# Optimization experiments

Measured on AMD Instinct MI355X. Metric: run time of the kernel, lower is better.

## Reference

```python
import jax, jax.numpy as jnp
import numpy as np

NUM_HEADS = 8
DIM_NODE, DIM_EDGE, DIM_TIME, DIM_OUT = 512, 172, 100, 512
U_NODE, U_EDGE, U_TIME, NUM_DST, E = 100000, 8192, 50000, 16384, 131072


def _linear_params(k, fan_in, fan_out):
    # torch.nn.Linear default init: U(-1/sqrt(fan_in), 1/sqrt(fan_in))
    kw, kb = jax.random.split(k)
    bound = 1.0 / np.sqrt(fan_in)
    w = jax.random.uniform(kw, (fan_in, fan_out), jnp.float32, -bound, bound)
    b = jax.random.uniform(kb, (fan_out,), jnp.float32, -bound, bound)
    return w, b


def setup_inputs() -> dict:
    key = jax.random.key(0)
    ks = jax.random.split(key, 16)
    inp = {}
    inp["idx"] = jax.random.randint(ks[0], (E,), 0, NUM_DST, jnp.int32)
    inp["nodeData"] = jax.random.normal(ks[1], (U_NODE, DIM_NODE), jnp.float32)
    inp["node_inverse"] = jax.random.randint(ks[2], (E,), 0, U_NODE, jnp.int32)
    inp["node_dst_inverse"] = jax.random.randint(ks[3], (NUM_DST,), 0, U_NODE, jnp.int32)
    inp["efeat_unique"] = jax.random.normal(ks[4], (U_EDGE, DIM_EDGE), jnp.float32)
    inp["efeat_inverse"] = jax.random.randint(ks[5], (E,), 0, U_EDGE, jnp.int32)
    inp["time_unique"] = jax.random.normal(ks[6], (U_TIME, DIM_TIME), jnp.float32)
    inp["time_inverse"] = jax.random.randint(ks[7], (E,), 0, U_TIME, jnp.int32)
    inp["time_dst_unique"] = jax.random.normal(ks[8], (1, DIM_TIME), jnp.float32)
    inp["time_dst_inverse"] = jnp.zeros((NUM_DST,), jnp.int32)
    inp["wq_node_w"], inp["wq_node_b"] = _linear_params(ks[9], DIM_NODE, DIM_OUT)
    inp["wq_time_w"], inp["wq_time_b"] = _linear_params(ks[10], DIM_TIME, DIM_OUT)
    inp["wkv_node_w"], inp["wkv_node_b"] = _linear_params(ks[11], DIM_NODE, 2 * DIM_OUT)
    inp["wkv_edge_w"], inp["wkv_edge_b"] = _linear_params(ks[12], DIM_EDGE, 2 * DIM_OUT)
    inp["wkv_time_w"], inp["wkv_time_b"] = _linear_params(ks[13], DIM_TIME, 2 * DIM_OUT)
    return inp


def reference(idx, nodeData, node_inverse, node_dst_inverse, efeat_unique,
              efeat_inverse, time_unique, time_inverse, time_dst_unique,
              time_dst_inverse, wq_node_w, wq_node_b, wq_time_w, wq_time_b,
              wkv_node_w, wkv_node_b, wkv_edge_w, wkv_edge_b, wkv_time_w,
              wkv_time_b):
    # project on UNIQUE rows, then scatter via inverse indices (dedup pattern)
    q_node = (nodeData @ wq_node_w + wq_node_b)[node_dst_inverse]      # [num_dst, D]
    q_time = (time_dst_unique @ wq_time_w + wq_time_b)[time_dst_inverse]
    Q = (q_node + q_time)[idx]                                          # [E, D]
    z_node = (nodeData @ wkv_node_w + wkv_node_b)[node_inverse]         # [E, 2D]
    z_edge = (efeat_unique @ wkv_edge_w + wkv_edge_b)[efeat_inverse]
    z_time = (time_unique @ wkv_time_w + wkv_time_b)[time_inverse]
    Z = z_node + z_edge + z_time
    D = wq_node_w.shape[1]
    K, V = Z[:, :D], Z[:, D:]
    n = Q.shape[0]
    Qh = Q.reshape(n, NUM_HEADS, -1)
    Kh = K.reshape(n, NUM_HEADS, -1)
    Vh = V.reshape(n, NUM_HEADS, -1)
    attn = jnp.sum(Qh * Kh, axis=2)                                      # [E, H]
    attn = jnp.where(attn >= 0, attn, 0.2 * attn)                        # LeakyReLU(0.2)
    return attn, Vh
```

## Files before the change

### kernel.cpp

```cpp
#include <hip/hip_runtime.h>
#include <hip/hip_bf16.h>

typedef __bf16 bf16_t;
typedef __bf16 bf16x8 __attribute__((ext_vector_type(8)));
typedef float  f32x4  __attribute__((ext_vector_type(4)));

#define E_NUM   131072
#define NDST    16384
#define DN      512
#define DE      172
#define DEP     192
#define DT      100
#define DTP     128
#define DO      512
#define KTOT    832
#define VBASE   (E_NUM * 8)

typedef const __attribute__((address_space(1))) char gbl_t;
typedef __attribute__((address_space(3))) char lds_t;

#define GLOAD_LDS16(g, l) __builtin_amdgcn_global_load_lds((gbl_t*)(g), (lds_t*)(l), 16, 0, 0)

__global__ void cvt_bf16_vec(const float* __restrict__ src, bf16_t* __restrict__ dst, long n8) {
    long i = (long)blockIdx.x * blockDim.x + threadIdx.x;
    long stride = (long)gridDim.x * blockDim.x;
    for (; i < n8; i += stride) {
        const float4* p = reinterpret_cast<const float4*>(src + i * 8);
        float4 a = p[0], b = p[1];
        union { bf16_t h[8]; uint4 q; } t;
        t.h[0]=(bf16_t)a.x; t.h[1]=(bf16_t)a.y; t.h[2]=(bf16_t)a.z; t.h[3]=(bf16_t)a.w;
        t.h[4]=(bf16_t)b.x; t.h[5]=(bf16_t)b.y; t.h[6]=(bf16_t)b.z; t.h[7]=(bf16_t)b.w;
        *reinterpret_cast<uint4*>(dst + i * 8) = t.q;
    }
}

__global__ void cvt_pad(const float* __restrict__ src, bf16_t* __restrict__ dst,
                        int rows, int cin, int cout) {
    long total = (long)rows * cout;
    long i = (long)blockIdx.x * blockDim.x + threadIdx.x;
    long stride = (long)gridDim.x * blockDim.x;
    for (; i < total; i += stride) {
        int r = (int)(i / cout), c = (int)(i - (long)r * cout);
        dst[i] = (c < cin) ? (bf16_t)src[(size_t)r * cin + c] : (bf16_t)0.0f;
    }
}

__global__ void prep_wkvT(const float* __restrict__ wn, const float* __restrict__ we,
                          const float* __restrict__ wt, const float* __restrict__ bn,
                          const float* __restrict__ be, const float* __restrict__ bt,
                          bf16_t* __restrict__ WkvT, float* __restrict__ kvbias) {
    int n = blockIdx.x;
    for (int k = threadIdx.x; k < KTOT; k += blockDim.x) {
        float v;
        if (k < 512)            v = wn[(size_t)k * 1024 + n];
        else if (k < 512 + DE)  v = we[(size_t)(k - 512) * 1024 + n];
        else if (k < 704)       v = 0.0f;
        else if (k < 704 + DT)  v = wt[(size_t)(k - 704) * 1024 + n];
        else                    v = 0.0f;
        WkvT[(size_t)n * KTOT + k] = (bf16_t)v;
    }
    if (threadIdx.x == 0) kvbias[n] = bn[n] + be[n] + bt[n];
}

__global__ void prep_wqT(const float* __restrict__ wq, bf16_t* __restrict__ WqT) {
    int n = blockIdx.x;
    for (int k = threadIdx.x; k < DO; k += blockDim.x)
        WqT[(size_t)n * DO + k] = (bf16_t)wq[(size_t)k * DO + n];
}

__global__ void prep_qbias(const float* __restrict__ td, const float* __restrict__ wqt,
                           const float* __restrict__ bqt, const float* __restrict__ bqn,
                           float* __restrict__ qbias) {
    int n = blockIdx.x * blockDim.x + threadIdx.x;
    if (n < DO) {
        float s = bqt[n] + bqn[n];
        for (int k = 0; k < DT; ++k) s += td[k] * wqt[(size_t)k * DO + n];
        qbias[n] = s;
    }
}

__global__ __launch_bounds__(256) void qd_gemm_kernel(
    const bf16_t* __restrict__ node_bf, const int* __restrict__ node_dst,
    const bf16_t* __restrict__ WqT, const float* __restrict__ qbias,
    float* __restrict__ QD) {
    const int bx = blockIdx.x;
    const int mt = bx >> 2, nt = bx & 3;
    const int d0 = mt * 128, n0 = nt * 128;
    const int tid = threadIdx.x;
    const int lane = tid & 63, wid = tid >> 6;
    const int wm = wid >> 1, wn = wid & 1;
    const int lr = lane & 15, lg = lane >> 4;

    __shared__ __align__(16) bf16_t Ash[2][128 * 32];
    __shared__ __align__(16) bf16_t Bsh[2][128 * 32];

    const int srow = wid * 32 + (lane >> 2);
    const int achk = lane & 3;
    const bf16_t* pa0 = node_bf + (size_t)node_dst[d0 + srow] * DN + achk * 8;
    const bf16_t* pa1 = node_bf + (size_t)node_dst[d0 + srow + 16] * DN + achk * 8;
    const bf16_t* pb0 = WqT + (size_t)(n0 + srow) * DO + achk * 8;
    const bf16_t* pb1 = pb0 + (size_t)16 * DO;

#define QD_STAGE(buf, kt) do {                                                   \
        int k0_ = (kt) * 32;                                                     \
        GLOAD_LDS16(pa0 + k0_, &Ash[buf][0] + wid * 1024);                       \
        GLOAD_LDS16(pa1 + k0_, &Ash[buf][0] + wid * 1024 + 512);                 \
        GLOAD_LDS16(pb0 + k0_, &Bsh[buf][0] + wid * 1024);                       \
        GLOAD_LDS16(pb1 + k0_, &Bsh[buf][0] + wid * 1024 + 512);                 \
    } while (0)

    f32x4 acc[4][4];
#pragma unroll
    for (int i = 0; i < 4; ++i)
#pragma unroll
        for (int j = 0; j < 4; ++j) { acc[i][j][0]=0.f; acc[i][j][1]=0.f; acc[i][j][2]=0.f; acc[i][j][3]=0.f; }

    QD_STAGE(0, 0);
    __syncthreads();
    int cur = 0;
    for (int kt = 0; kt < 16; ++kt) {
        if (kt < 15) QD_STAGE(cur ^ 1, kt + 1);
        bf16x8 af[4], bfr[4];
#pragma unroll
        for (int mi = 0; mi < 4; ++mi)
            af[mi] = *reinterpret_cast<const bf16x8*>(&Ash[cur][(wm * 64 + mi * 16 + lr) * 32 + lg * 8]);
#pragma unroll
        for (int ni = 0; ni < 4; ++ni)
            bfr[ni] = *reinterpret_cast<const bf16x8*>(&Bsh[cur][(wn * 64 + ni * 16 + lr) * 32 + lg * 8]);
#pragma unroll
        for (int mi = 0; mi < 4; ++mi)
#pragma unroll
            for (int ni = 0; ni < 4; ++ni)
                acc[mi][ni] = __builtin_amdgcn_mfma_f32_16x16x32_bf16(af[mi], bfr[ni], acc[mi][ni], 0, 0, 0);
        __syncthreads();
        cur ^= 1;
    }

    float qb[4];
#pragma unroll
    for (int ni = 0; ni < 4; ++ni) qb[ni] = qbias[n0 + wn * 64 + ni * 16 + lr];
#pragma unroll
    for (int mi = 0; mi < 4; ++mi)
#pragma unroll
        for (int j = 0; j < 4; ++j) {
            int m = wm * 64 + mi * 16 + lg * 4 + j;
            float* op = QD + (size_t)(d0 + m) * DO + n0 + wn * 64 + lr;
#pragma unroll
            for (int ni = 0; ni < 4; ++ni) op[ni * 16] = acc[mi][ni][j] + qb[ni];
        }
#undef QD_STAGE
}

__global__ __launch_bounds__(512) void kv_attn_kernel(
    const bf16_t* __restrict__ node_bf, const bf16_t* __restrict__ edge_bf,
    const bf16_t* __restrict__ time_bf, const int* __restrict__ node_inverse,
    const int* __restrict__ efeat_inverse, const int* __restrict__ time_inverse,
    const int* __restrict__ idx, const bf16_t* __restrict__ WkvT,
    const float* __restrict__ kvbias, const float* __restrict__ QD,
    float* __restrict__ out) {
    const int bx = blockIdx.x;
    const int mt = bx >> 2, nt = bx & 3;
    const int e0 = mt * 128, n0 = nt * 256;
    const int tid = threadIdx.x;
    const int lane = tid & 63, wid = tid >> 6;
    const int wm = wid >> 2, wn = wid & 3;
    const int lr = lane & 15, lg = lane >> 4;

    __shared__ __align__(16) bf16_t Ash[2][128 * 32];
    __shared__ __align__(16) bf16_t Bsh[2][256 * 32];
    __shared__ int qrow_s[128];

    if (tid < 128) qrow_s[tid] = idx[e0 + tid];

    const int arow = wid * 16 + (lane >> 2);
    const int achk = lane & 3;
    const int ae = e0 + arow;
    const bf16_t* pn = node_bf + (size_t)node_inverse[ae] * DN  + achk * 8;
    const bf16_t* pe = edge_bf + (size_t)efeat_inverse[ae] * DEP + achk * 8;
    const bf16_t* pt = time_bf + (size_t)time_inverse[ae] * DTP + achk * 8;
    const int brow = wid * 32 + (lane >> 2);
    const bf16_t* pb0 = WkvT + (size_t)(n0 + brow) * KTOT + achk * 8;
    const bf16_t* pb1 = pb0 + (size_t)16 * KTOT;

#define KV_STAGE(buf, kt) do {                                                   \
        int k0_ = (kt) * 32;                                                     \
        const bf16_t* ga_;                                                       \
        if (k0_ < 512)      ga_ = pn + k0_;                                      \
        else if (k0_ < 704) ga_ = pe + (k0_ - 512);                              \
        else                ga_ = pt + (k0_ - 704);                              \
        GLOAD_LDS16(ga_,       &Ash[buf][0] + wid * 512);                        \
        GLOAD_LDS16(pb0 + k0_, &Bsh[buf][0] + wid * 1024);                       \
        GLOAD_LDS16(pb1 + k0_, &Bsh[buf][0] + wid * 1024 + 512);                 \
    } while (0)

    f32x4 acc[4][4];
#pragma unroll
    for (int i = 0; i < 4; ++i)
#pragma unroll
        for (int j = 0; j < 4; ++j) { acc[i][j][0]=0.f; acc[i][j][1]=0.f; acc[i][j][2]=0.f; acc[i][j][3]=0.f; }

    KV_STAGE(0, 0);
    __syncthreads();
    int cur = 0;
    for (int kt = 0; kt < 26; ++kt) {
        if (kt < 25) KV_STAGE(cur ^ 1, kt + 1);
        bf16x8 af[4], bfr[4];
#pragma unroll
        for (int mi = 0; mi < 4; ++mi)
            af[mi] = *reinterpret_cast<const bf16x8*>(&Ash[cur][(wm * 64 + mi * 16 + lr) * 32 + lg * 8]);
#pragma unroll
        for (int ni = 0; ni < 4; ++ni)
            bfr[ni] = *reinterpret_cast<const bf16x8*>(&Bsh[cur][(wn * 64 + ni * 16 + lr) * 32 + lg * 8]);
#pragma unroll
        for (int mi = 0; mi < 4; ++mi)
#pragma unroll
            for (int ni = 0; ni < 4; ++ni)
                acc[mi][ni] = __builtin_amdgcn_mfma_f32_16x16x32_bf16(af[mi], bfr[ni], acc[mi][ni], 0, 0, 0);
        __syncthreads();
        cur ^= 1;
    }
#undef KV_STAGE

    float kvb[4];
#pragma unroll
    for (int ni = 0; ni < 4; ++ni) kvb[ni] = kvbias[n0 + wn * 64 + ni * 16 + lr];

    if (nt < 2) {
        const int head = nt * 4 + wn;
        const int hcol = head * 64;
        float p[4][4];
#pragma unroll
        for (int mi = 0; mi < 4; ++mi)
#pragma unroll
            for (int j = 0; j < 4; ++j) {
                int m = wm * 64 + mi * 16 + lg * 4 + j;
                int qr = qrow_s[m];
                const float* qp = QD + (size_t)qr * DO + hcol + lr;
                float s = 0.f;
#pragma unroll
                for (int ni = 0; ni < 4; ++ni)
                    s += (acc[mi][ni][j] + kvb[ni]) * qp[ni * 16];
                p[mi][j] = s;
            }
#pragma unroll
        for (int off = 1; off < 16; off <<= 1)
#pragma unroll
            for (int mi = 0; mi < 4; ++mi)
#pragma unroll
                for (int j = 0; j < 4; ++j)
                    p[mi][j] += __shfl_xor(p[mi][j], off, 64);
        if (lr == 0) {
#pragma unroll
            for (int mi = 0; mi < 4; ++mi)
#pragma unroll
                for (int j = 0; j < 4; ++j) {
                    int e = e0 + wm * 64 + mi * 16 + lg * 4 + j;
                    float s = p[mi][j];
                    out[(size_t)e * 8 + head] = (s >= 0.f) ? s : 0.2f * s;
                }
        }
    } else {
        const int vcol0 = n0 - 512 + wn * 64;
#pragma unroll
        for (int mi = 0; mi < 4; ++mi)
#pragma unroll
            for (int j = 0; j < 4; ++j) {
                int e = e0 + wm * 64 + mi * 16 + lg * 4 + j;
                float* op = out + VBASE + (size_t)e * 512 + vcol0 + lr;
#pragma unroll
                for (int ni = 0; ni < 4; ++ni) op[ni * 16] = acc[mi][ni][j] + kvb[ni];
            }
    }
}

extern "C" void kernel_launch(void* const* d_in, const int* in_sizes, int n_in,
                              void* d_out, int out_size, void* d_ws, size_t ws_size,
                              hipStream_t stream) {
    const int*   idx        = (const int*)d_in[0];
    const float* nodeData   = (const float*)d_in[1];
    const int*   node_inv   = (const int*)d_in[2];
    const int*   node_dst   = (const int*)d_in[3];
    const float* efeat      = (const float*)d_in[4];
    const int*   efeat_inv  = (const int*)d_in[5];
    const float* time_u     = (const float*)d_in[6];
    const int*   time_inv   = (const int*)d_in[7];
    const float* time_dst   = (const float*)d_in[8];
    const float* wq_node_w  = (const float*)d_in[10];
    const float* wq_node_b  = (const float*)d_in[11];
    const float* wq_time_w  = (const float*)d_in[12];
    const float* wq_time_b  = (const float*)d_in[13];
    const float* wkv_node_w = (const float*)d_in[14];
    const float* wkv_node_b = (const float*)d_in[15];
    const float* wkv_edge_w = (const float*)d_in[16];
    const float* wkv_edge_b = (const float*)d_in[17];
    const float* wkv_time_w = (const float*)d_in[18];
    const float* wkv_time_b = (const float*)d_in[19];

    char* ws = (char*)d_ws;
    bf16_t* node_bf = (bf16_t*)(ws + 0);
    bf16_t* edge_bf = (bf16_t*)(ws + 102400000);
    bf16_t* time_bf = (bf16_t*)(ws + 105545728);
    bf16_t* WkvT    = (bf16_t*)(ws + 118345728);
    bf16_t* WqT     = (bf16_t*)(ws + 120049664);
    float*  kvbias  = (float*)(ws + 120573952);
    float*  qbias   = (float*)(ws + 120578048);
    float*  QD      = (float*)(ws + 120580096);
    float*  out     = (float*)d_out;

    cvt_bf16_vec<<<2048, 256, 0, stream>>>(nodeData, node_bf, (long)100000 * 512 / 8);
    cvt_pad<<<512, 256, 0, stream>>>(efeat, edge_bf, 8192, DE, DEP);
    cvt_pad<<<1024, 256, 0, stream>>>(time_u, time_bf, 50000, DT, DTP);
    prep_wkvT<<<1024, 256, 0, stream>>>(wkv_node_w, wkv_edge_w, wkv_time_w,
                                        wkv_node_b, wkv_edge_b, wkv_time_b, WkvT, kvbias);
    prep_wqT<<<512, 256, 0, stream>>>(wq_node_w, WqT);
    prep_qbias<<<2, 256, 0, stream>>>(time_dst, wq_time_w, wq_time_b, wq_node_b, qbias);
    qd_gemm_kernel<<<512, 256, 0, stream>>>(node_bf, node_dst, WqT, qbias, QD);
    kv_attn_kernel<<<4096, 512, 0, stream>>>(node_bf, edge_bf, time_bf, node_inv,
                                             efeat_inv, time_inv, idx, WkvT, kvbias, QD, out);
}
```

Measured before the change: 428.3 us.

## Swizzle LDS chunk layout and remap block order in both GEMM kernels

Global-to-LDS loads now place each 16-byte K-chunk at a rotated position that depends on the row, and the fragment reads use the matching rotated index. This is meant to remove LDS bank conflicts on the row-strided fragment reads. Block indices are also permuted so that consecutive blocks are spread across 8 groups, likely aiming for better XCD/L2 locality for the shared weight tiles. The risk is that the permutation assumes particular grid sizes (512 and 4096 blocks), and a swizzle mismatch would corrupt results.

```diff
diff --git a/kernel.cpp b/kernel.cpp
--- a/kernel.cpp
+++ b/kernel.cpp
@@ -83,7 +83,7 @@
     const bf16_t* __restrict__ node_bf, const int* __restrict__ node_dst,
     const bf16_t* __restrict__ WqT, const float* __restrict__ qbias,
     float* __restrict__ QD) {
-    const int bx = blockIdx.x;
+    const int bx = ((blockIdx.x & 7) << 6) + (blockIdx.x >> 3);
     const int mt = bx >> 2, nt = bx & 3;
     const int d0 = mt * 128, n0 = nt * 128;
     const int tid = threadIdx.x;
@@ -95,10 +95,10 @@
     __shared__ __align__(16) bf16_t Bsh[2][128 * 32];
 
     const int srow = wid * 32 + (lane >> 2);
-    const int achk = lane & 3;
-    const bf16_t* pa0 = node_bf + (size_t)node_dst[d0 + srow] * DN + achk * 8;
-    const bf16_t* pa1 = node_bf + (size_t)node_dst[d0 + srow + 16] * DN + achk * 8;
-    const bf16_t* pb0 = WqT + (size_t)(n0 + srow) * DO + achk * 8;
+    const int csrc = ((lane & 3) - ((lane >> 3) & 3)) & 3;
+    const bf16_t* pa0 = node_bf + (size_t)node_dst[d0 + srow] * DN + csrc * 8;
+    const bf16_t* pa1 = node_bf + (size_t)node_dst[d0 + srow + 16] * DN + csrc * 8;
+    const bf16_t* pb0 = WqT + (size_t)(n0 + srow) * DO + csrc * 8;
     const bf16_t* pb1 = pb0 + (size_t)16 * DO;
 
 #define QD_STAGE(buf, kt) do {                                                   \
@@ -115,6 +115,8 @@
 #pragma unroll
         for (int j = 0; j < 4; ++j) { acc[i][j][0]=0.f; acc[i][j][1]=0.f; acc[i][j][2]=0.f; acc[i][j][3]=0.f; }
 
+    const int rchk = ((lg + (lr >> 1)) & 3) * 8;
+
     QD_STAGE(0, 0);
     __syncthreads();
     int cur = 0;
@@ -123,10 +125,10 @@
         bf16x8 af[4], bfr[4];
 #pragma unroll
         for (int mi = 0; mi < 4; ++mi)
-            af[mi] = *reinterpret_cast<const bf16x8*>(&Ash[cur][(wm * 64 + mi * 16 + lr) * 32 + lg * 8]);
+            af[mi] = *reinterpret_cast<const bf16x8*>(&Ash[cur][(wm * 64 + mi * 16 + lr) * 32 + rchk]);
 #pragma unroll
         for (int ni = 0; ni < 4; ++ni)
-            bfr[ni] = *reinterpret_cast<const bf16x8*>(&Bsh[cur][(wn * 64 + ni * 16 + lr) * 32 + lg * 8]);
+            bfr[ni] = *reinterpret_cast<const bf16x8*>(&Bsh[cur][(wn * 64 + ni * 16 + lr) * 32 + rchk]);
 #pragma unroll
         for (int mi = 0; mi < 4; ++mi)
 #pragma unroll
@@ -158,7 +160,7 @@
     const int* __restrict__ idx, const bf16_t* __restrict__ WkvT,
     const float* __restrict__ kvbias, const float* __restrict__ QD,
     float* __restrict__ out) {
-    const int bx = blockIdx.x;
+    const int bx = ((blockIdx.x & 7) << 9) + (blockIdx.x >> 3);
     const int mt = bx >> 2, nt = bx & 3;
     const int e0 = mt * 128, n0 = nt * 256;
     const int tid = threadIdx.x;
@@ -172,14 +174,14 @@
 
     if (tid < 128) qrow_s[tid] = idx[e0 + tid];
 
+    const int csrc = ((lane & 3) - ((lane >> 3) & 3)) & 3;
     const int arow = wid * 16 + (lane >> 2);
-    const int achk = lane & 3;
     const int ae = e0 + arow;
-    const bf16_t* pn = node_bf + (size_t)node_inverse[ae] * DN  + achk * 8;
-    const bf16_t* pe = edge_bf + (size_t)efeat_inverse[ae] * DEP + achk * 8;
-    const bf16_t* pt = time_bf + (size_t)time_inverse[ae] * DTP + achk * 8;
+    const bf16_t* pn = node_bf + (size_t)node_inverse[ae] * DN  + csrc * 8;
+    const bf16_t* pe = edge_bf + (size_t)efeat_inverse[ae] * DEP + csrc * 8;
+    const bf16_t* pt = time_bf + (size_t)time_inverse[ae] * DTP + csrc * 8;
     const int brow = wid * 32 + (lane >> 2);
-    const bf16_t* pb0 = WkvT + (size_t)(n0 + brow) * KTOT + achk * 8;
+    const bf16_t* pb0 = WkvT + (size_t)(n0 + brow) * KTOT + csrc * 8;
     const bf16_t* pb1 = pb0 + (size_t)16 * KTOT;
 
 #define KV_STAGE(buf, kt) do {                                                   \
@@ -199,6 +201,8 @@
 #pragma unroll
         for (int j = 0; j < 4; ++j) { acc[i][j][0]=0.f; acc[i][j][1]=0.f; acc[i][j][2]=0.f; acc[i][j][3]=0.f; }
 
+    const int rchk = ((lg + (lr >> 1)) & 3) * 8;
+
     KV_STAGE(0, 0);
     __syncthreads();
     int cur = 0;
@@ -207,10 +211,10 @@
         bf16x8 af[4], bfr[4];
 #pragma unroll
         for (int mi = 0; mi < 4; ++mi)
-            af[mi] = *reinterpret_cast<const bf16x8*>(&Ash[cur][(wm * 64 + mi * 16 + lr) * 32 + lg * 8]);
+            af[mi] = *reinterpret_cast<const bf16x8*>(&Ash[cur][(wm * 64 + mi * 16 + lr) * 32 + rchk]);
 #pragma unroll
         for (int ni = 0; ni < 4; ++ni)
-            bfr[ni] = *reinterpret_cast<const bf16x8*>(&Bsh[cur][(wn * 64 + ni * 16 + lr) * 32 + lg * 8]);
+            bfr[ni] = *reinterpret_cast<const bf16x8*>(&Bsh[cur][(wn * 64 + ni * 16 + lr) * 32 + rchk]);
 #pragma unroll
         for (int mi = 0; mi < 4; ++mi)
 #pragma unroll
```

New measurement: 407.7 us, median of 2. 4.8% less time.
